# Kernel tuning notes

Hardware: AMD Instinct MI355X
Metric: run time of the kernel (lower is better)

The kernel has to match this reference:

```python
import jax, jax.numpy as jnp
import numpy as np

WS = 8      # window_size
SS = 4      # shift_size
NH = 16     # num_heads


def _rel_position_index(ws):
    # matches WindowMSA.double_step_seq + flip(1)
    seq1 = np.arange(0, (2 * ws - 1) * ws, 2 * ws - 1)
    seq2 = np.arange(0, ws)
    rel = (seq1[:, None] + seq2[None, :]).reshape(1, -1)  # (1, ws*ws)
    idx = rel + rel.T                                      # (ws*ws, ws*ws)
    return np.ascontiguousarray(idx[:, ::-1]).astype(np.int32)


def _shift_attn_mask(H, W, ws, ss):
    # static numpy construction of the Swin shift mask, (nW, N, N)
    img = np.zeros((H, W), dtype=np.int32)
    slices = (slice(0, -ws), slice(-ws, -ss), slice(-ss, None))
    cnt = 0
    for h in slices:
        for w in slices:
            img[h, w] = cnt
            cnt += 1
    win = img.reshape(H // ws, ws, W // ws, ws).transpose(0, 2, 1, 3).reshape(-1, ws * ws)
    diff = win[:, None, :] - win[:, :, None]
    return np.where(diff != 0, -100.0, 0.0).astype(np.float32)


def setup_inputs() -> dict:
    key = jax.random.key(0)
    ks = jax.random.split(key, 6)
    B, H, W, C = 16, 64, 64, 512
    return {
        "query": jax.random.normal(ks[0], (B, H * W, C), jnp.float32),
        "qkv_w": jax.random.normal(ks[1], (3 * C, C), jnp.float32) * 0.02,
        "qkv_b": jnp.zeros((3 * C,), jnp.float32),
        "proj_w": jax.random.normal(ks[2], (C, C), jnp.float32) * 0.02,
        "proj_b": jnp.zeros((C,), jnp.float32),
        "bias_table": jax.random.normal(ks[3], ((2 * WS - 1) ** 2, NH), jnp.float32) * 0.02,
        "rel_index": jnp.asarray(_rel_position_index(WS)),
        "H": H,
        "W": W,
    }


def reference(query, qkv_w, qkv_b, proj_w, proj_b, bias_table, rel_index, H, W):
    B, L, C = query.shape
    hd = C // NH
    scale = hd ** -0.5
    N = WS * WS
    nW = (H // WS) * (W // WS)

    x = query.reshape(B, H, W, C)
    # cyclic shift
    x = jnp.roll(x, (-SS, -SS), axis=(1, 2))
    # window partition -> (B*nW, N, C)
    xw = x.reshape(B, H // WS, WS, W // WS, WS, C).transpose(0, 1, 3, 2, 4, 5)
    xw = xw.reshape(B * nW, N, C)

    # qkv projection
    qkv = xw @ qkv_w.T + qkv_b                       # (BnW, N, 3C)
    qkv = qkv.reshape(B * nW, N, 3, NH, hd).transpose(2, 0, 3, 1, 4)
    q, k, v = qkv[0], qkv[1], qkv[2]                 # (BnW, NH, N, hd)

    attn = jnp.einsum('whnd,whmd->whnm', q * scale, k)

    # relative position bias (N, N, NH) -> (NH, N, N)
    bias = bias_table[rel_index.reshape(-1)].reshape(N, N, NH).transpose(2, 0, 1)
    attn = attn + bias[None]

    # shift mask (static)
    mask = jnp.asarray(_shift_attn_mask(H, W, WS, SS))  # (nW, N, N)
    attn = attn.reshape(B, nW, NH, N, N) + mask[None, :, None]
    attn = jax.nn.softmax(attn.reshape(B * nW, NH, N, N), axis=-1)

    out = jnp.einsum('whnm,whmd->whnd', attn, v)     # (BnW, NH, N, hd)
    out = out.transpose(0, 2, 1, 3).reshape(B * nW, N, C)
    out = out @ proj_w.T + proj_b

    # window reverse -> (B, H, W, C)
    out = out.reshape(B, H // WS, W // WS, WS, WS, C).transpose(0, 1, 3, 2, 4, 5)
    out = out.reshape(B, H, W, C)
    # reverse cyclic shift
    out = jnp.roll(out, (SS, SS), axis=(1, 2))
    return out.reshape(B, H * W, C)
```

## Files before the change

### kernel.cpp

```cpp
#include <hip/hip_runtime.h>


typedef short  short8  __attribute__((ext_vector_type(8)));
typedef short  short4v __attribute__((ext_vector_type(4)));
typedef float  floatx4 __attribute__((ext_vector_type(4)));

#define DEVI static __device__ __forceinline__

DEVI unsigned short f2bf(float f) {
    union { float f; unsigned int u; } v;
    v.f = f;
    return (unsigned short)((v.u + 0x7fffu + ((v.u >> 16) & 1u)) >> 16);
}

__global__ void wcvt(const float* __restrict__ qkv_w,
                     const float* __restrict__ proj_w,
                     unsigned short* __restrict__ wbf) {
    const int idx = ((blockIdx.x << 8) + threadIdx.x) << 2;
    const float* src = (idx < 786432) ? (qkv_w + idx) : (proj_w + (idx - 786432));
    const floatx4 v = *(const floatx4*)src;
    short4v o;
    o[0] = (short)f2bf(v[0]); o[1] = (short)f2bf(v[1]);
    o[2] = (short)f2bf(v[2]); o[3] = (short)f2bf(v[3]);
    *(short4v*)(wbf + idx) = o;
}

__global__ void xcvt(const float* __restrict__ query,
                     unsigned short* __restrict__ xw) {
    const int bid = blockIdx.x;
    const int x   = bid & 7;
    const int s   = bid >> 3;
    const int win = (x << 7) + (s >> 4);
    const int rem = ((s & 15) << 8) + threadIdx.x;
    const int jc  = rem & 3;
    const int tok = (rem >> 2) & 63;
    const int kc  = rem >> 8;
    const int b   = win >> 6, wy = (win >> 3) & 7, wx = win & 7;
    const int ty  = tok >> 3, tx = tok & 7;
    const int gh  = ((wy << 3) + ty + 4) & 63;
    const int gw  = ((wx << 3) + tx + 4) & 63;
    const float* src = query + (((b << 12) + (gh << 6) + gw) << 9) + (kc << 5) + (jc << 3);
    const floatx4 v0 = *(const floatx4*)src;
    const floatx4 v1 = *(const floatx4*)(src + 4);
    short8 sv;
    sv[0] = (short)f2bf(v0[0]); sv[1] = (short)f2bf(v0[1]);
    sv[2] = (short)f2bf(v0[2]); sv[3] = (short)f2bf(v0[3]);
    sv[4] = (short)f2bf(v1[0]); sv[5] = (short)f2bf(v1[1]);
    sv[6] = (short)f2bf(v1[2]); sv[7] = (short)f2bf(v1[3]);
    *(short8*)(xw + (win << 15) + (kc << 11) + (tok << 5) + (jc << 3)) = sv;
}

__global__ __launch_bounds__(256, 2)
void k_fused(const unsigned short* __restrict__ wbf,
             const unsigned short* __restrict__ xw,
             const float* __restrict__ qkv_b,
             const float* __restrict__ proj_b,
             const float* __restrict__ bias_table,
             float* __restrict__ out)
{
    __shared__ __align__(16) unsigned short smem[33280];

    const int tid  = threadIdx.x;
    const int lane = tid & 63;
    const int l15  = lane & 15;
    const int quad = lane >> 4;
    const int wave = tid >> 6;

    const int win = blockIdx.x;
    const int b   = win >> 6;
    const int wy  = (win >> 3) & 7;
    const int wx  = win & 7;
    const int mid = ((wy == 7) ? 2 : 0) | ((wx == 7) ? 1 : 0);

    unsigned short* xs  = smem;
    unsigned short* wb  = smem + wave * 7424;
    unsigned short* qbf = wb;
    unsigned short* kbf = wb + 2560;
    unsigned short* vT  = wb + 5120;
    unsigned short* pbf = wb;

    const unsigned short* xa = xw + (win << 15) + (l15 << 5) + (quad << 3);
    const float scale = 0.17677669529663687f;
    const floatx4 fz = {0.f, 0.f, 0.f, 0.f};
    unsigned int po[4][16];

    for (int hh = 0; hh < 4; ++hh) {
        const int h = (wave << 2) + hh;
        floatx4 accq[4][2], acck[4][2], accv[4][2];
        #pragma unroll
        for (int mt = 0; mt < 4; ++mt)
            #pragma unroll
            for (int nt = 0; nt < 2; ++nt) { accq[mt][nt] = fz; acck[mt][nt] = fz; accv[mt][nt] = fz; }

        const unsigned short* wq = wbf + ((h << 5) + l15) * 512 + (quad << 3);
        const unsigned short* wk = wq + 262144;
        const unsigned short* wv = wk + 262144;

        short8 a_c[4], bq_c[2], bk_c[2], bv_c[2];
        #pragma unroll
        for (int mt = 0; mt < 4; ++mt)
            a_c[mt] = *(const short8*)(xa + (mt << 9));
        #pragma unroll
        for (int nt = 0; nt < 2; ++nt) {
            const int ro = (nt << 4) * 512;
            bq_c[nt] = *(const short8*)(wq + ro);
            bk_c[nt] = *(const short8*)(wk + ro);
            bv_c[nt] = *(const short8*)(wv + ro);
        }
        #pragma unroll 2
        for (int kk = 0; kk < 512; kk += 32) {
            const int kn = (kk + 32) & 511;
            short8 a_n[4], bq_n[2], bk_n[2], bv_n[2];
            #pragma unroll
            for (int mt = 0; mt < 4; ++mt)
                a_n[mt] = *(const short8*)(xa + (kn << 6) + (mt << 9));
            #pragma unroll
            for (int nt = 0; nt < 2; ++nt) {
                const int ro = (nt << 4) * 512 + kn;
                bq_n[nt] = *(const short8*)(wq + ro);
                bk_n[nt] = *(const short8*)(wk + ro);
                bv_n[nt] = *(const short8*)(wv + ro);
            }
            #pragma unroll
            for (int nt = 0; nt < 2; ++nt)
                #pragma unroll
                for (int mt = 0; mt < 4; ++mt) {
                    accq[mt][nt] = __builtin_amdgcn_mfma_f32_16x16x32_bf16(a_c[mt], bq_c[nt], accq[mt][nt], 0, 0, 0);
                    acck[mt][nt] = __builtin_amdgcn_mfma_f32_16x16x32_bf16(a_c[mt], bk_c[nt], acck[mt][nt], 0, 0, 0);
                    accv[mt][nt] = __builtin_amdgcn_mfma_f32_16x16x32_bf16(a_c[mt], bv_c[nt], accv[mt][nt], 0, 0, 0);
                }
            #pragma unroll
            for (int mt = 0; mt < 4; ++mt) a_c[mt] = a_n[mt];
            #pragma unroll
            for (int nt = 0; nt < 2; ++nt) {
                bq_c[nt] = bq_n[nt]; bk_c[nt] = bk_n[nt]; bv_c[nt] = bv_n[nt];
            }
        }

        #pragma unroll
        for (int nt = 0; nt < 2; ++nt) {
            const int cix = (h << 5) + (nt << 4) + l15;
            const float bq_ = qkv_b[cix];
            const float bk_ = qkv_b[512 + cix];
            const float bv_ = qkv_b[1024 + cix];
            #pragma unroll
            for (int mt = 0; mt < 4; ++mt) {
                short4v vv;
                #pragma unroll
                for (int r = 0; r < 4; ++r) {
                    const int row = (mt << 4) + (quad << 2) + r;
                    qbf[row * 40 + (nt << 4) + l15] = f2bf(accq[mt][nt][r] + bq_);
                    kbf[row * 40 + (nt << 4) + l15] = f2bf(acck[mt][nt][r] + bk_);
                    vv[r] = (short)f2bf(accv[mt][nt][r] + bv_);
                }
                *(short4v*)&vT[((nt << 4) + l15) * 72 + (mt << 4) + (quad << 2)] = vv;
            }
        }

        short8 qa[4], ka[4];
        #pragma unroll
        for (int t = 0; t < 4; ++t) {
            qa[t] = *(const short8*)&qbf[((t << 4) + l15) * 40 + (quad << 3)];
            ka[t] = *(const short8*)&kbf[((t << 4) + l15) * 40 + (quad << 3)];
        }
        floatx4 s4[4][4];
        #pragma unroll
        for (int mt = 0; mt < 4; ++mt)
            #pragma unroll
            for (int nt = 0; nt < 4; ++nt)
                s4[mt][nt] = __builtin_amdgcn_mfma_f32_16x16x32_bf16(qa[mt], ka[nt], fz, 0, 0, 0);

        int  gjv[4]; bool jrow[4], jcol[4];
        #pragma unroll
        for (int nt = 0; nt < 4; ++nt) {
            const int j  = (nt << 4) + l15;
            const int j2 = 63 - j;
            gjv[nt]  = 15 * (j2 >> 3) + (j2 & 7);
            jrow[nt] = (j >> 3) < 4;
            jcol[nt] = (j & 7) < 4;
        }
        #pragma unroll
        for (int mt = 0; mt < 4; ++mt) {
            const int i0  = (mt << 4) + (quad << 2);
            const int fi0 = 15 * (i0 >> 3) + (i0 & 7);
            const bool irow = (i0 >> 3) < 4;
            const bool icol = (i0 & 7) == 0;
            #pragma unroll
            for (int nt = 0; nt < 4; ++nt) {
                float mval = 0.0f;
                if ((mid & 2) && (irow != jrow[nt])) mval = -100.0f;
                if ((mid & 1) && (icol != jcol[nt])) mval = -100.0f;
                const float* bp = bias_table + (fi0 + gjv[nt]) * 16 + h;
                #pragma unroll
                for (int r = 0; r < 4; ++r)
                    s4[mt][nt][r] = s4[mt][nt][r] * scale + bp[r * 16] + mval;
            }
        }

        #pragma unroll
        for (int mt = 0; mt < 4; ++mt)
            #pragma unroll
            for (int r = 0; r < 4; ++r) {
                float m = fmaxf(fmaxf(s4[mt][0][r], s4[mt][1][r]),
                                fmaxf(s4[mt][2][r], s4[mt][3][r]));
                m = fmaxf(m, __shfl_xor(m, 1));
                m = fmaxf(m, __shfl_xor(m, 2));
                m = fmaxf(m, __shfl_xor(m, 4));
                m = fmaxf(m, __shfl_xor(m, 8));
                float loc = 0.0f;
                #pragma unroll
                for (int nt = 0; nt < 4; ++nt) {
                    s4[mt][nt][r] = __expf(s4[mt][nt][r] - m);
                    loc += s4[mt][nt][r];
                }
                loc += __shfl_xor(loc, 1);
                loc += __shfl_xor(loc, 2);
                loc += __shfl_xor(loc, 4);
                loc += __shfl_xor(loc, 8);
                const float inv = 1.0f / loc;
                const int row = (mt << 4) + (quad << 2) + r;
                #pragma unroll
                for (int nt = 0; nt < 4; ++nt)
                    pbf[row * 72 + (nt << 4) + l15] = f2bf(s4[mt][nt][r] * inv);
            }

        short8 pa[4][2], va[2][2];
        #pragma unroll
        for (int mt = 0; mt < 4; ++mt)
            #pragma unroll
            for (int ks = 0; ks < 2; ++ks)
                pa[mt][ks] = *(const short8*)&pbf[((mt << 4) + l15) * 72 + (ks << 5) + (quad << 3)];
        #pragma unroll
        for (int nt = 0; nt < 2; ++nt)
            #pragma unroll
            for (int ks = 0; ks < 2; ++ks)
                va[nt][ks] = *(const short8*)&vT[((nt << 4) + l15) * 72 + (ks << 5) + (quad << 3)];

        #pragma unroll
        for (int mt = 0; mt < 4; ++mt)
            #pragma unroll
            for (int nt = 0; nt < 2; ++nt) {
                floatx4 acc = fz;
                acc = __builtin_amdgcn_mfma_f32_16x16x32_bf16(pa[mt][0], va[nt][0], acc, 0, 0, 0);
                acc = __builtin_amdgcn_mfma_f32_16x16x32_bf16(pa[mt][1], va[nt][1], acc, 0, 0, 0);
                const int pi = ((mt << 1) + nt) << 1;
                po[hh][pi]     = (unsigned int)f2bf(acc[0]) | ((unsigned int)f2bf(acc[1]) << 16);
                po[hh][pi + 1] = (unsigned int)f2bf(acc[2]) | ((unsigned int)f2bf(acc[3]) << 16);
            }
    }
    __syncthreads();

    #pragma unroll
    for (int hh = 0; hh < 4; ++hh) {
        const int ch0 = (((wave << 2) + hh) << 5) + l15;
        #pragma unroll
        for (int mt = 0; mt < 4; ++mt)
            #pragma unroll
            for (int nt = 0; nt < 2; ++nt) {
                const int pi = ((mt << 1) + nt) << 1;
                #pragma unroll
                for (int r = 0; r < 4; ++r) {
                    const int row = (mt << 4) + (quad << 2) + r;
                    const unsigned int w = po[hh][pi + (r >> 1)];
                    xs[row * 520 + ch0 + (nt << 4)] =
                        (unsigned short)((w >> ((r & 1) << 4)) & 0xffffu);
                }
            }
    }
    __syncthreads();

    const unsigned short* pwb = wbf + 786432;
    for (int pass = 0; pass < 2; ++pass) {
        const int co0 = (wave << 7) + (pass << 6);
        floatx4 acc[4][4];
        #pragma unroll
        for (int mt = 0; mt < 4; ++mt)
            #pragma unroll
            for (int nt = 0; nt < 4; ++nt) acc[mt][nt] = fz;

        const unsigned short* wp = pwb + (co0 + l15) * 512 + (quad << 3);

        short8 bf_c[4];
        #pragma unroll
        for (int nt = 0; nt < 4; ++nt)
            bf_c[nt] = *(const short8*)(wp + (nt << 4) * 512);

        #pragma unroll 2
        for (int kk = 0; kk < 512; kk += 32) {
            const int kn = (kk + 32) & 511;
            short8 a[4], bf_n[4];
            #pragma unroll
            for (int nt = 0; nt < 4; ++nt)
                bf_n[nt] = *(const short8*)(wp + (nt << 4) * 512 + kn);
            #pragma unroll
            for (int mt = 0; mt < 4; ++mt)
                a[mt] = *(const short8*)&xs[((mt << 4) + l15) * 520 + kk + (quad << 3)];
            #pragma unroll
            for (int nt = 0; nt < 4; ++nt)
                #pragma unroll
                for (int mt = 0; mt < 4; ++mt)
                    acc[mt][nt] = __builtin_amdgcn_mfma_f32_16x16x32_bf16(a[mt], bf_c[nt], acc[mt][nt], 0, 0, 0);
            #pragma unroll
            for (int nt = 0; nt < 4; ++nt) bf_c[nt] = bf_n[nt];
        }

        #pragma unroll
        for (int nt = 0; nt < 4; ++nt) {
            const float pb_ = proj_b[co0 + (nt << 4) + l15];
            #pragma unroll
            for (int mt = 0; mt < 4; ++mt)
                #pragma unroll
                for (int r = 0; r < 4; ++r) {
                    const int tok = (mt << 4) + (quad << 2) + r;
                    const int ty = tok >> 3, tx = tok & 7;
                    const int gh = ((wy << 3) + ty + 4) & 63;
                    const int gw = ((wx << 3) + tx + 4) & 63;
                    out[(((b << 12) + (gh << 6) + gw) << 9) + co0 + (nt << 4) + l15] =
                        acc[mt][nt][r] + pb_;
                }
        }
    }
}

__global__ __launch_bounds__(256, 1)
void k_legacy(const float* __restrict__ query,
              const unsigned short* __restrict__ wbf,
              const float* __restrict__ qkv_b,
              const float* __restrict__ proj_b,
              const float* __restrict__ bias_table,
              float* __restrict__ out)
{
    __shared__ __align__(16) unsigned short smem[62976];

    const int tid  = threadIdx.x;
    const int lane = tid & 63;
    const int l15  = lane & 15;
    const int quad = lane >> 4;
    const int wave = tid >> 6;

    const int win = blockIdx.x;
    const int b   = win >> 6;
    const int wy  = (win >> 3) & 7;
    const int wx  = win & 7;
    const int mid = ((wy == 7) ? 2 : 0) | ((wx == 7) ? 1 : 0);

    unsigned short* xs  = smem;
    unsigned short* wb  = smem + 33280 + wave * 7424;
    unsigned short* qbf = wb;
    unsigned short* kbf = wb + 2560;
    unsigned short* vT  = wb + 5120;
    unsigned short* pbf = wb;

    #pragma unroll
    for (int it = 0; it < 32; ++it) {
        const int c   = tid + (it << 8);
        const int tok = c >> 7;
        const int fo  = (c & 127) << 2;
        const int ty  = tok >> 3, tx = tok & 7;
        const int gh  = ((wy << 3) + ty + 4) & 63;
        const int gw  = ((wx << 3) + tx + 4) & 63;
        const floatx4 v = *(const floatx4*)(query + (((b << 12) + (gh << 6) + gw) << 9) + fo);
        short4v s;
        s[0] = (short)f2bf(v[0]); s[1] = (short)f2bf(v[1]);
        s[2] = (short)f2bf(v[2]); s[3] = (short)f2bf(v[3]);
        *(short4v*)&xs[tok * 520 + fo] = s;
    }
    __syncthreads();

    const float scale = 0.17677669529663687f;
    const floatx4 fz = {0.f, 0.f, 0.f, 0.f};
    unsigned int po[4][16];

    for (int hh = 0; hh < 4; ++hh) {
        const int h = (wave << 2) + hh;
        floatx4 accq[4][2], acck[4][2], accv[4][2];
        #pragma unroll
        for (int mt = 0; mt < 4; ++mt)
            #pragma unroll
            for (int nt = 0; nt < 2; ++nt) { accq[mt][nt] = fz; acck[mt][nt] = fz; accv[mt][nt] = fz; }

        const unsigned short* wq = wbf + ((h << 5) + l15) * 512 + (quad << 3);
        const unsigned short* wk = wq + 262144;
        const unsigned short* wv = wk + 262144;

        #pragma unroll 2
        for (int kk = 0; kk < 512; kk += 32) {
            short8 a[4], bq[2], bk2[2], bv2[2];
            #pragma unroll
            for (int mt = 0; mt < 4; ++mt)
                a[mt] = *(const short8*)&xs[((mt << 4) + l15) * 520 + kk + (quad << 3)];
            #pragma unroll
            for (int nt = 0; nt < 2; ++nt) {
                const int ro = (nt << 4) * 512 + kk;
                bq[nt]  = *(const short8*)(wq + ro);
                bk2[nt] = *(const short8*)(wk + ro);
                bv2[nt] = *(const short8*)(wv + ro);
            }
            #pragma unroll
            for (int nt = 0; nt < 2; ++nt)
                #pragma unroll
                for (int mt = 0; mt < 4; ++mt) {
                    accq[mt][nt] = __builtin_amdgcn_mfma_f32_16x16x32_bf16(a[mt], bq[nt],  accq[mt][nt], 0, 0, 0);
                    acck[mt][nt] = __builtin_amdgcn_mfma_f32_16x16x32_bf16(a[mt], bk2[nt], acck[mt][nt], 0, 0, 0);
                    accv[mt][nt] = __builtin_amdgcn_mfma_f32_16x16x32_bf16(a[mt], bv2[nt], accv[mt][nt], 0, 0, 0);
                }
        }

        #pragma unroll
        for (int nt = 0; nt < 2; ++nt) {
            const int cix = (h << 5) + (nt << 4) + l15;
            const float bq_ = qkv_b[cix];
            const float bk_ = qkv_b[512 + cix];
            const float bv_ = qkv_b[1024 + cix];
            #pragma unroll
            for (int mt = 0; mt < 4; ++mt) {
                short4v vv;
                #pragma unroll
                for (int r = 0; r < 4; ++r) {
                    const int row = (mt << 4) + (quad << 2) + r;
                    qbf[row * 40 + (nt << 4) + l15] = f2bf(accq[mt][nt][r] + bq_);
                    kbf[row * 40 + (nt << 4) + l15] = f2bf(acck[mt][nt][r] + bk_);
                    vv[r] = (short)f2bf(accv[mt][nt][r] + bv_);
                }
                *(short4v*)&vT[((nt << 4) + l15) * 72 + (mt << 4) + (quad << 2)] = vv;
            }
        }

        short8 qa[4], ka[4];
        #pragma unroll
        for (int t = 0; t < 4; ++t) {
            qa[t] = *(const short8*)&qbf[((t << 4) + l15) * 40 + (quad << 3)];
            ka[t] = *(const short8*)&kbf[((t << 4) + l15) * 40 + (quad << 3)];
        }
        floatx4 s4[4][4];
        #pragma unroll
        for (int mt = 0; mt < 4; ++mt)
            #pragma unroll
            for (int nt = 0; nt < 4; ++nt)
                s4[mt][nt] = __builtin_amdgcn_mfma_f32_16x16x32_bf16(qa[mt], ka[nt], fz, 0, 0, 0);

        int  gjv[4]; bool jrow[4], jcol[4];
        #pragma unroll
        for (int nt = 0; nt < 4; ++nt) {
            const int j  = (nt << 4) + l15;
            const int j2 = 63 - j;
            gjv[nt]  = 15 * (j2 >> 3) + (j2 & 7);
            jrow[nt] = (j >> 3) < 4;
            jcol[nt] = (j & 7) < 4;
        }
        #pragma unroll
        for (int mt = 0; mt < 4; ++mt) {
            const int i0  = (mt << 4) + (quad << 2);
            const int fi0 = 15 * (i0 >> 3) + (i0 & 7);
            const bool irow = (i0 >> 3) < 4;
            const bool icol = (i0 & 7) == 0;
            #pragma unroll
            for (int nt = 0; nt < 4; ++nt) {
                float mval = 0.0f;
                if ((mid & 2) && (irow != jrow[nt])) mval = -100.0f;
                if ((mid & 1) && (icol != jcol[nt])) mval = -100.0f;
                const float* bp = bias_table + (fi0 + gjv[nt]) * 16 + h;
                #pragma unroll
                for (int r = 0; r < 4; ++r)
                    s4[mt][nt][r] = s4[mt][nt][r] * scale + bp[r * 16] + mval;
            }
        }

        #pragma unroll
        for (int mt = 0; mt < 4; ++mt)
            #pragma unroll
            for (int r = 0; r < 4; ++r) {
                float m = fmaxf(fmaxf(s4[mt][0][r], s4[mt][1][r]),
                                fmaxf(s4[mt][2][r], s4[mt][3][r]));
                m = fmaxf(m, __shfl_xor(m, 1));
                m = fmaxf(m, __shfl_xor(m, 2));
                m = fmaxf(m, __shfl_xor(m, 4));
                m = fmaxf(m, __shfl_xor(m, 8));
                float loc = 0.0f;
                #pragma unroll
                for (int nt = 0; nt < 4; ++nt) {
                    s4[mt][nt][r] = __expf(s4[mt][nt][r] - m);
                    loc += s4[mt][nt][r];
                }
                loc += __shfl_xor(loc, 1);
                loc += __shfl_xor(loc, 2);
                loc += __shfl_xor(loc, 4);
                loc += __shfl_xor(loc, 8);
                const float inv = 1.0f / loc;
                const int row = (mt << 4) + (quad << 2) + r;
                #pragma unroll
                for (int nt = 0; nt < 4; ++nt)
                    pbf[row * 72 + (nt << 4) + l15] = f2bf(s4[mt][nt][r] * inv);
            }

        short8 pa[4][2], va[2][2];
        #pragma unroll
        for (int mt = 0; mt < 4; ++mt)
            #pragma unroll
            for (int ks = 0; ks < 2; ++ks)
                pa[mt][ks] = *(const short8*)&pbf[((mt << 4) + l15) * 72 + (ks << 5) + (quad << 3)];
        #pragma unroll
        for (int nt = 0; nt < 2; ++nt)
            #pragma unroll
            for (int ks = 0; ks < 2; ++ks)
                va[nt][ks] = *(const short8*)&vT[((nt << 4) + l15) * 72 + (ks << 5) + (quad << 3)];

        #pragma unroll
        for (int mt = 0; mt < 4; ++mt)
            #pragma unroll
            for (int nt = 0; nt < 2; ++nt) {
                floatx4 acc = fz;
                acc = __builtin_amdgcn_mfma_f32_16x16x32_bf16(pa[mt][0], va[nt][0], acc, 0, 0, 0);
                acc = __builtin_amdgcn_mfma_f32_16x16x32_bf16(pa[mt][1], va[nt][1], acc, 0, 0, 0);
                const int pi = ((mt << 1) + nt) << 1;
                po[hh][pi]     = (unsigned int)f2bf(acc[0]) | ((unsigned int)f2bf(acc[1]) << 16);
                po[hh][pi + 1] = (unsigned int)f2bf(acc[2]) | ((unsigned int)f2bf(acc[3]) << 16);
            }
    }
    __syncthreads();

    #pragma unroll
    for (int hh = 0; hh < 4; ++hh) {
        const int ch0 = (((wave << 2) + hh) << 5) + l15;
        #pragma unroll
        for (int mt = 0; mt < 4; ++mt)
            #pragma unroll
            for (int nt = 0; nt < 2; ++nt) {
                const int pi = ((mt << 1) + nt) << 1;
                #pragma unroll
                for (int r = 0; r < 4; ++r) {
                    const int row = (mt << 4) + (quad << 2) + r;
                    const unsigned int w = po[hh][pi + (r >> 1)];
                    xs[row * 520 + ch0 + (nt << 4)] =
                        (unsigned short)((w >> ((r & 1) << 4)) & 0xffffu);
                }
            }
    }
    __syncthreads();

    const unsigned short* pwb = wbf + 786432;
    for (int pass = 0; pass < 2; ++pass) {
        const int co0 = (wave << 7) + (pass << 6);
        floatx4 acc[4][4];
        #pragma unroll
        for (int mt = 0; mt < 4; ++mt)
            #pragma unroll
            for (int nt = 0; nt < 4; ++nt) acc[mt][nt] = fz;

        const unsigned short* wp = pwb + (co0 + l15) * 512 + (quad << 3);

        #pragma unroll 2
        for (int kk = 0; kk < 512; kk += 32) {
            short8 a[4], bfr[4];
            #pragma unroll
            for (int mt = 0; mt < 4; ++mt)
                a[mt] = *(const short8*)&xs[((mt << 4) + l15) * 520 + kk + (quad << 3)];
            #pragma unroll
            for (int nt = 0; nt < 4; ++nt)
                bfr[nt] = *(const short8*)(wp + (nt << 4) * 512 + kk);
            #pragma unroll
            for (int nt = 0; nt < 4; ++nt)
                #pragma unroll
                for (int mt = 0; mt < 4; ++mt)
                    acc[mt][nt] = __builtin_amdgcn_mfma_f32_16x16x32_bf16(a[mt], bfr[nt], acc[mt][nt], 0, 0, 0);
        }

        #pragma unroll
        for (int nt = 0; nt < 4; ++nt) {
            const float pb_ = proj_b[co0 + (nt << 4) + l15];
            #pragma unroll
            for (int mt = 0; mt < 4; ++mt)
                #pragma unroll
                for (int r = 0; r < 4; ++r) {
                    const int tok = (mt << 4) + (quad << 2) + r;
                    const int ty = tok >> 3, tx = tok & 7;
                    const int gh = ((wy << 3) + ty + 4) & 63;
                    const int gw = ((wx << 3) + tx + 4) & 63;
                    out[(((b << 12) + (gh << 6) + gw) << 9) + co0 + (nt << 4) + l15] =
                        acc[mt][nt][r] + pb_;
                }
        }
    }
}

extern "C" void kernel_launch(void* const* d_in, const int* in_sizes, int n_in,
                              void* d_out, int out_size, void* d_ws, size_t ws_size,
                              hipStream_t stream) {
    const float* query      = (const float*)d_in[0];
    const float* qkv_w      = (const float*)d_in[1];
    const float* qkv_b      = (const float*)d_in[2];
    const float* proj_w     = (const float*)d_in[3];
    const float* proj_b     = (const float*)d_in[4];
    const float* bias_table = (const float*)d_in[5];

    unsigned short* wbf = (unsigned short*)d_ws;
    unsigned short* xw  = wbf + 1048576;

    const size_t needB = (size_t)(1048576 + 33554432) * sizeof(unsigned short);

    if (ws_size >= needB) {
        hipLaunchKernelGGL(wcvt,    dim3(1024),  dim3(256), 0, stream, qkv_w, proj_w, wbf);
        hipLaunchKernelGGL(xcvt,    dim3(16384), dim3(256), 0, stream, query, xw);
        hipLaunchKernelGGL(k_fused, dim3(1024),  dim3(256), 0, stream,
                           wbf, xw, qkv_b, proj_b, bias_table, (float*)d_out);
    } else {
        hipLaunchKernelGGL(wcvt,     dim3(1024), dim3(256), 0, stream, qkv_w, proj_w, wbf);
        hipLaunchKernelGGL(k_legacy, dim3(1024), dim3(256), 0, stream,
                           query, wbf, qkv_b, proj_b, bias_table, (float*)d_out);
    }
}
```

Measured before the change: 419.3 us.

## Shrink LDS via XOR-swizzled q/k/v/p tiles and split projection staging into halves

Replaces padded LDS row strides for the per-wave q, k, vT and p tiles with unpadded XOR-swizzled layouts. The projection input is staged in two 256-channel rounds instead of a full 512-channel buffer, so total shared memory drops from about 65KB to 48KB, which may let more blocks fit per CU. It also removes the explicit register double-buffering of global loads in the QKV GEMM and the projection loop. That lowers register pressure but exposes more load latency, and it adds extra barriers for the two staging rounds.

```diff
diff --git a/kernel.cpp b/kernel.cpp
--- a/kernel.cpp
+++ b/kernel.cpp
@@ -51,14 +51,14 @@
 }
 
 __global__ __launch_bounds__(256, 2)
-void k_fused(const unsigned short* __restrict__ wbf,
-             const unsigned short* __restrict__ xw,
-             const float* __restrict__ qkv_b,
-             const float* __restrict__ proj_b,
-             const float* __restrict__ bias_table,
-             float* __restrict__ out)
+void k_fused3(const unsigned short* __restrict__ wbf,
+              const unsigned short* __restrict__ xw,
+              const float* __restrict__ qkv_b,
+              const float* __restrict__ proj_b,
+              const float* __restrict__ bias_table,
+              float* __restrict__ out)
 {
-    __shared__ __align__(16) unsigned short smem[33280];
+    __shared__ __align__(16) unsigned short smem[24576];
 
     const int tid  = threadIdx.x;
     const int lane = tid & 63;
@@ -72,20 +72,24 @@
     const int wx  = win & 7;
     const int mid = ((wy == 7) ? 2 : 0) | ((wx == 7) ? 1 : 0);
 
-    unsigned short* xs  = smem;
-    unsigned short* wb  = smem + wave * 7424;
-    unsigned short* qbf = wb;
-    unsigned short* kbf = wb + 2560;
-    unsigned short* vT  = wb + 5120;
-    unsigned short* pbf = wb;
+    unsigned short* wbs = smem + wave * 6144;
+    unsigned short* qbf = wbs;
+    unsigned short* kbf = wbs + 2048;
+    unsigned short* vT  = wbs + 4096;
+    unsigned short* pbf = wbs;
+
+    const int sw4 = (l15 & 3) ^ (l15 >> 2);
+    const int sw8 = (l15 & 7) ^ (l15 >> 3);
 
     const unsigned short* xa = xw + (win << 15) + (l15 << 5) + (quad << 3);
     const float scale = 0.17677669529663687f;
     const floatx4 fz = {0.f, 0.f, 0.f, 0.f};
+
     unsigned int po[4][16];
 
     for (int hh = 0; hh < 4; ++hh) {
         const int h = (wave << 2) + hh;
+
         floatx4 accq[4][2], acck[4][2], accv[4][2];
         #pragma unroll
         for (int mt = 0; mt < 4; ++mt)
@@ -96,45 +100,27 @@
         const unsigned short* wk = wq + 262144;
         const unsigned short* wv = wk + 262144;
 
-        short8 a_c[4], bq_c[2], bk_c[2], bv_c[2];
-        #pragma unroll
-        for (int mt = 0; mt < 4; ++mt)
-            a_c[mt] = *(const short8*)(xa + (mt << 9));
-        #pragma unroll
-        for (int nt = 0; nt < 2; ++nt) {
-            const int ro = (nt << 4) * 512;
-            bq_c[nt] = *(const short8*)(wq + ro);
-            bk_c[nt] = *(const short8*)(wk + ro);
-            bv_c[nt] = *(const short8*)(wv + ro);
-        }
         #pragma unroll 2
         for (int kk = 0; kk < 512; kk += 32) {
-            const int kn = (kk + 32) & 511;
-            short8 a_n[4], bq_n[2], bk_n[2], bv_n[2];
+            short8 a[4], bq[2], bk2[2], bv2[2];
             #pragma unroll
             for (int mt = 0; mt < 4; ++mt)
-                a_n[mt] = *(const short8*)(xa + (kn << 6) + (mt << 9));
+                a[mt] = *(const short8*)(xa + (kk << 6) + (mt << 9));
             #pragma unroll
             for (int nt = 0; nt < 2; ++nt) {
-                const int ro = (nt << 4) * 512 + kn;
-                bq_n[nt] = *(const short8*)(wq + ro);
-                bk_n[nt] = *(const short8*)(wk + ro);
-                bv_n[nt] = *(const short8*)(wv + ro);
+                const int ro = (nt << 4) * 512 + kk;
+                bq[nt]  = *(const short8*)(wq + ro);
+                bk2[nt] = *(const short8*)(wk + ro);
+                bv2[nt] = *(const short8*)(wv + ro);
             }
             #pragma unroll
             for (int nt = 0; nt < 2; ++nt)
                 #pragma unroll
                 for (int mt = 0; mt < 4; ++mt) {
-                    accq[mt][nt] = __builtin_amdgcn_mfma_f32_16x16x32_bf16(a_c[mt], bq_c[nt], accq[mt][nt], 0, 0, 0);
-                    acck[mt][nt] = __builtin_amdgcn_mfma_f32_16x16x32_bf16(a_c[mt], bk_c[nt], acck[mt][nt], 0, 0, 0);
-                    accv[mt][nt] = __builtin_amdgcn_mfma_f32_16x16x32_bf16(a_c[mt], bv_c[nt], accv[mt][nt], 0, 0, 0);
-                }
-            #pragma unroll
-            for (int mt = 0; mt < 4; ++mt) a_c[mt] = a_n[mt];
-            #pragma unroll
-            for (int nt = 0; nt < 2; ++nt) {
-                bq_c[nt] = bq_n[nt]; bk_c[nt] = bk_n[nt]; bv_c[nt] = bv_n[nt];
-            }
+                    accq[mt][nt] = __builtin_amdgcn_mfma_f32_16x16x32_bf16(a[mt], bq[nt],  accq[mt][nt], 0, 0, 0);
+                    acck[mt][nt] = __builtin_amdgcn_mfma_f32_16x16x32_bf16(a[mt], bk2[nt], acck[mt][nt], 0, 0, 0);
+                    accv[mt][nt] = __builtin_amdgcn_mfma_f32_16x16x32_bf16(a[mt], bv2[nt], accv[mt][nt], 0, 0, 0);
+                }
         }
 
         #pragma unroll
@@ -149,19 +135,23 @@
                 #pragma unroll
                 for (int r = 0; r < 4; ++r) {
                     const int row = (mt << 4) + (quad << 2) + r;
-                    qbf[row * 40 + (nt << 4) + l15] = f2bf(accq[mt][nt][r] + bq_);
-                    kbf[row * 40 + (nt << 4) + l15] = f2bf(acck[mt][nt][r] + bk_);
+                    const int ph  = (2 * nt + (l15 >> 3)) ^ (row & 3) ^ ((row >> 2) & 3);
+                    const int off = (row << 5) + (l15 & 7) + (ph << 3);
+                    qbf[off] = f2bf(accq[mt][nt][r] + bq_);
+                    kbf[off] = f2bf(acck[mt][nt][r] + bk_);
                     vv[r] = (short)f2bf(accv[mt][nt][r] + bv_);
                 }
-                *(short4v*)&vT[((nt << 4) + l15) * 72 + (mt << 4) + (quad << 2)] = vv;
+                const int vph = (2 * mt + (quad >> 1)) ^ sw8;
+                *(short4v*)&vT[(((nt << 4) + l15) << 6) + ((quad & 1) << 2) + (vph << 3)] = vv;
             }
         }
 
         short8 qa[4], ka[4];
         #pragma unroll
         for (int t = 0; t < 4; ++t) {
-            qa[t] = *(const short8*)&qbf[((t << 4) + l15) * 40 + (quad << 3)];
-            ka[t] = *(const short8*)&kbf[((t << 4) + l15) * 40 + (quad << 3)];
+            const int off = ((((t << 4) + l15)) << 5) + ((quad ^ sw4) << 3);
+            qa[t] = *(const short8*)&qbf[off];
+            ka[t] = *(const short8*)&kbf[off];
         }
         floatx4 s4[4][4];
         #pragma unroll
@@ -220,8 +210,10 @@
                 const float inv = 1.0f / loc;
                 const int row = (mt << 4) + (quad << 2) + r;
                 #pragma unroll
-                for (int nt = 0; nt < 4; ++nt)
-                    pbf[row * 72 + (nt << 4) + l15] = f2bf(s4[mt][nt][r] * inv);
+                for (int nt = 0; nt < 4; ++nt) {
+                    const int ph = (2 * nt + (l15 >> 3)) ^ (row & 7) ^ ((row >> 3) & 1);
+                    pbf[(row << 6) + (l15 & 7) + (ph << 3)] = f2bf(s4[mt][nt][r] * inv);
+                }
             }
 
         short8 pa[4][2], va[2][2];
@@ -229,12 +221,12 @@
         for (int mt = 0; mt < 4; ++mt)
             #pragma unroll
             for (int ks = 0; ks < 2; ++ks)
-                pa[mt][ks] = *(const short8*)&pbf[((mt << 4) + l15) * 72 + (ks << 5) + (quad << 3)];
+                pa[mt][ks] = *(const short8*)&pbf[((((mt << 4) + l15)) << 6) + ((((ks << 2) + quad) ^ sw8) << 3)];
         #pragma unroll
         for (int nt = 0; nt < 2; ++nt)
             #pragma unroll
             for (int ks = 0; ks < 2; ++ks)
-                va[nt][ks] = *(const short8*)&vT[((nt << 4) + l15) * 72 + (ks << 5) + (quad << 3)];
+                va[nt][ks] = *(const short8*)&vT[((((nt << 4) + l15)) << 6) + ((((ks << 2) + quad) ^ sw8) << 3)];
 
         #pragma unroll
         for (int mt = 0; mt < 4; ++mt)
@@ -248,28 +240,10 @@
                 po[hh][pi + 1] = (unsigned int)f2bf(acc[2]) | ((unsigned int)f2bf(acc[3]) << 16);
             }
     }
-    __syncthreads();
-
-    #pragma unroll
-    for (int hh = 0; hh < 4; ++hh) {
-        const int ch0 = (((wave << 2) + hh) << 5) + l15;
-        #pragma unroll
-        for (int mt = 0; mt < 4; ++mt)
-            #pragma unroll
-            for (int nt = 0; nt < 2; ++nt) {
-                const int pi = ((mt << 1) + nt) << 1;
-                #pragma unroll
-                for (int r = 0; r < 4; ++r) {
-                    const int row = (mt << 4) + (quad << 2) + r;
-                    const unsigned int w = po[hh][pi + (r >> 1)];
-                    xs[row * 520 + ch0 + (nt << 4)] =
-                        (unsigned short)((w >> ((r & 1) << 4)) & 0xffffu);
-                }
-            }
-    }
-    __syncthreads();
-
+
+    unsigned short* xsh = smem;
     const unsigned short* pwb = wbf + 786432;
+
     for (int pass = 0; pass < 2; ++pass) {
         const int co0 = (wave << 7) + (pass << 6);
         floatx4 acc[4][4];
@@ -278,30 +252,46 @@
             #pragma unroll
             for (int nt = 0; nt < 4; ++nt) acc[mt][nt] = fz;
 
-        const unsigned short* wp = pwb + (co0 + l15) * 512 + (quad << 3);
-
-        short8 bf_c[4];
-        #pragma unroll
-        for (int nt = 0; nt < 4; ++nt)
-            bf_c[nt] = *(const short8*)(wp + (nt << 4) * 512);
-
-        #pragma unroll 2
-        for (int kk = 0; kk < 512; kk += 32) {
-            const int kn = (kk + 32) & 511;
-            short8 a[4], bf_n[4];
-            #pragma unroll
-            for (int nt = 0; nt < 4; ++nt)
-                bf_n[nt] = *(const short8*)(wp + (nt << 4) * 512 + kn);
-            #pragma unroll
-            for (int mt = 0; mt < 4; ++mt)
-                a[mt] = *(const short8*)&xs[((mt << 4) + l15) * 520 + kk + (quad << 3)];
-            #pragma unroll
-            for (int nt = 0; nt < 4; ++nt)
+        const unsigned short* wp = pwb + (co0 + l15) * 512;
+
+        for (int rnd = 0; rnd < 2; ++rnd) {
+            __syncthreads();
+            #pragma unroll
+            for (int hi = 0; hi < 2; ++hi) {
+                const int hh = (rnd << 1) + hi;
+                const int c0 = (wave << 6) + (hi << 5) + l15;
                 #pragma unroll
                 for (int mt = 0; mt < 4; ++mt)
-                    acc[mt][nt] = __builtin_amdgcn_mfma_f32_16x16x32_bf16(a[mt], bf_c[nt], acc[mt][nt], 0, 0, 0);
-            #pragma unroll
-            for (int nt = 0; nt < 4; ++nt) bf_c[nt] = bf_n[nt];
+                    #pragma unroll
+                    for (int nt = 0; nt < 2; ++nt) {
+                        const int pi = ((mt << 1) + nt) << 1;
+                        #pragma unroll
+                        for (int r = 0; r < 4; ++r) {
+                            const int row = (mt << 4) + (quad << 2) + r;
+                            const unsigned int w = po[hh][pi + (r >> 1)];
+                            xsh[row * 264 + c0 + (nt << 4)] =
+                                (unsigned short)((w >> ((r & 1) << 4)) & 0xffffu);
+                        }
+                    }
+            }
+            __syncthreads();
+
+            #pragma unroll 2
+            for (int kk = 0; kk < 256; kk += 32) {
+                const int rb = ((kk >> 6) << 7) + (rnd << 6) + (kk & 63) + (quad << 3);
+                short8 a[4], bfr[4];
+                #pragma unroll
+                for (int mt = 0; mt < 4; ++mt)
+                    a[mt] = *(const short8*)&xsh[((mt << 4) + l15) * 264 + kk + (quad << 3)];
+                #pragma unroll
+                for (int nt = 0; nt < 4; ++nt)
+                    bfr[nt] = *(const short8*)(wp + (nt << 4) * 512 + rb);
+                #pragma unroll
+                for (int nt = 0; nt < 4; ++nt)
+                    #pragma unroll
+                    for (int mt = 0; mt < 4; ++mt)
+                        acc[mt][nt] = __builtin_amdgcn_mfma_f32_16x16x32_bf16(a[mt], bfr[nt], acc[mt][nt], 0, 0, 0);
+            }
         }
 
         #pragma unroll
@@ -599,9 +589,9 @@
     const size_t needB = (size_t)(1048576 + 33554432) * sizeof(unsigned short);
 
     if (ws_size >= needB) {
-        hipLaunchKernelGGL(wcvt,    dim3(1024),  dim3(256), 0, stream, qkv_w, proj_w, wbf);
-        hipLaunchKernelGGL(xcvt,    dim3(16384), dim3(256), 0, stream, query, xw);
-        hipLaunchKernelGGL(k_fused, dim3(1024),  dim3(256), 0, stream,
+        hipLaunchKernelGGL(wcvt,     dim3(1024),  dim3(256), 0, stream, qkv_w, proj_w, wbf);
+        hipLaunchKernelGGL(xcvt,     dim3(16384), dim3(256), 0, stream, query, xw);
+        hipLaunchKernelGGL(k_fused3, dim3(1024),  dim3(256), 0, stream,
                            wbf, xw, qkv_b, proj_b, bias_table, (float*)d_out);
     } else {
         hipLaunchKernelGGL(wcvt,     dim3(1024), dim3(256), 0, stream, qkv_w, proj_w, wbf);
```

Result: slower. 482.7 us (+15.1%).
